# Kernel optimization log

Measured on AMD Instinct MI355X. Metric: run time of the kernel, lower is better.

Reference implementation:

```python
import jax, jax.numpy as jnp
import numpy as np

BETA = 0.25


def setup_inputs() -> dict:
    key = jax.random.key(0)
    k1, k2 = jax.random.split(key)
    x = jax.random.normal(k1, (32768, 512), dtype=jnp.float32)
    centroids = jax.random.normal(k2, (8192, 512), dtype=jnp.float32)
    return {"x": x, "centroids": centroids}


def reference(x, centroids):
    # x: [N, D], centroids: [K, D]
    x_norm = jnp.sum(x * x, axis=1, keepdims=True)          # [N, 1]
    c_norm = jnp.sum(centroids * centroids, axis=1)         # [K]
    xy = jnp.einsum('nd,kd->nk', x, centroids)              # [N, K]
    distances = x_norm + c_norm[None, :] - 2.0 * xy         # [N, K]
    indices = jnp.argmin(distances, axis=-1)                # [N]
    q = centroids[indices]                                  # [N, D] gather
    # losses: commitment = mse(sg(q), x); codebook = mse(q, sg(x))
    sg = jax.lax.stop_gradient
    commitment_loss = jnp.mean((sg(q) - x) ** 2)
    codebook_loss = jnp.mean((q - sg(x)) ** 2)
    loss = codebook_loss + BETA * commitment_loss
    # straight-through estimator
    x_q = x + sg(q - x)
    return (x_q, loss, indices)
```

## Files before the change

kernel.cpp:

```cpp
#include <hip/hip_runtime.h>
#include <hip/hip_bf16.h>

#define N_ROWS 32768
#define DIM    512
#define K_CENT 8192

#define LOSS_OFF 16777216u
#define IDX_OFF  16777217u

#define XH_OFF_B   0u
#define CH_OFF_B   33554432u
#define CN_OFF_B   41943040u
#define CAND_OFF_B 41975808u

#define CAND_BYTES 2097152u
#define CN_BYTES   32768u

#define BM 128
#define BN 128
#define KHALF 4096
#define NKT (KHALF / BN)
#define NH  2

typedef __bf16 bf16x8 __attribute__((ext_vector_type(8)));
typedef float  f32x4  __attribute__((ext_vector_type(4)));

__device__ __forceinline__ unsigned short f2bf(float f) {
    unsigned u = __float_as_uint(f);
    return (unsigned short)((u + 0x7fffu + ((u >> 16) & 1u)) >> 16);
}

__device__ __forceinline__ void glds16(void* lds, const void* g) {
    __builtin_amdgcn_global_load_lds(
        (const __attribute__((address_space(1))) unsigned*)g,
        (__attribute__((address_space(3))) unsigned*)lds, 16, 0, 0);
}

__device__ __forceinline__ void ce(float& da, int& ia, float& db, int& ib) {
    bool sw = (db < da) || (db == da && ib < ia);
    float td = sw ? db : da; int ti = sw ? ib : ia;
    float ud = sw ? da : db; int ui = sw ? ia : ib;
    da = td; ia = ti; db = ud; ib = ui;
}
__device__ __forceinline__ void lmin(float da, int ia, float db, int ib,
                                     float& od, int& oi) {
    bool sw = (db < da) || (db == da && ib < ia);
    od = sw ? db : da; oi = sw ? ib : ia;
}

__global__ void __launch_bounds__(256) convert_kernel(const float* __restrict__ x,
                                                      const float* __restrict__ c,
                                                      unsigned short* __restrict__ xh,
                                                      unsigned short* __restrict__ ch,
                                                      float* __restrict__ cnp) {
    const int wave = threadIdx.x >> 6, lane = threadIdx.x & 63;
    const int gid = blockIdx.x * 4 + wave;
    if (gid < N_ROWS) {
        const float* p = x + (size_t)gid * DIM + lane * 8;
        float4 a = *(const float4*)p, b = *(const float4*)(p + 4);
        uint4 w;
        w.x = (unsigned)f2bf(a.x) | ((unsigned)f2bf(a.y) << 16);
        w.y = (unsigned)f2bf(a.z) | ((unsigned)f2bf(a.w) << 16);
        w.z = (unsigned)f2bf(b.x) | ((unsigned)f2bf(b.y) << 16);
        w.w = (unsigned)f2bf(b.z) | ((unsigned)f2bf(b.w) << 16);
        *(uint4*)(xh + (size_t)gid * DIM + lane * 8) = w;
    } else {
        const int cr = gid - N_ROWS;
        const float* p = c + (size_t)cr * DIM + lane * 8;
        float4 a = *(const float4*)p, b = *(const float4*)(p + 4);
        uint4 w;
        w.x = (unsigned)f2bf(a.x) | ((unsigned)f2bf(a.y) << 16);
        w.y = (unsigned)f2bf(a.z) | ((unsigned)f2bf(a.w) << 16);
        w.z = (unsigned)f2bf(b.x) | ((unsigned)f2bf(b.y) << 16);
        w.w = (unsigned)f2bf(b.z) | ((unsigned)f2bf(b.w) << 16);
        *(uint4*)(ch + (size_t)cr * DIM + lane * 8) = w;
        float s = a.x*a.x + a.y*a.y + a.z*a.z + a.w*a.w
                + b.x*b.x + b.y*b.y + b.z*b.z + b.w*b.w;
#pragma unroll
        for (int off = 32; off; off >>= 1) s += __shfl_down(s, off, 64);
        if (lane == 0) cnp[cr] = s;
    }
}

__global__ void __launch_bounds__(256, 2) vq_main(const unsigned short* __restrict__ xh,
                                                  const unsigned short* __restrict__ ch,
                                                  const float* __restrict__ cnp,
                                                  float* __restrict__ cand) {
    __shared__ __align__(16) unsigned short xs[4 * 4096];
    __shared__ __align__(16) unsigned short cs[4 * 4096];
    __shared__ float sh_d[2][BM][4];
    __shared__ int   sh_i[2][BM][4];

    const int tid  = threadIdx.x;
    const int wave = tid >> 6, lane = tid & 63;
    const int wm   = wave >> 1, wk = wave & 1;
    const int lr   = lane & 15, quad = lane >> 4;
    const int nbase = blockIdx.x * BM;
    const int h     = blockIdx.y;
    const int kc0   = h * KHALF;

    const int srow16 = lane >> 2;
    const int sswz   = (lane & 3) ^ ((lane >> 3) & 3);
    const unsigned short* xg0 = xh + (size_t)(nbase + wave * 32 + srow16) * DIM + sswz * 8;
    const unsigned short* xg1 = xg0 + (size_t)16 * DIM;
    const unsigned short* cg0 = ch + (size_t)(kc0 + wave * 32 + srow16) * DIM + sswz * 8;

    unsigned short* xw = xs + wave * 1024;
    unsigned short* cw = cs + wave * 1024;

#define STAGE(ring, ktn, dd) do {                                          \
        unsigned short* xd_ = xw + (ring) * 4096;                          \
        unsigned short* cd_ = cw + (ring) * 4096;                          \
        const unsigned short* cgk_ = cg0 + (size_t)(ktn) * (BN * DIM) + (dd); \
        glds16(xd_,       xg0 + (dd));                                     \
        glds16(xd_ + 512, xg1 + (dd));                                     \
        glds16(cd_,       cgk_);                                           \
        glds16(cd_ + 512, cgk_ + 16 * DIM);                                \
    } while (0)

    int aoff[4], boff[4];
#pragma unroll
    for (int t = 0; t < 4; ++t) {
        const int sw = (quad ^ ((lr >> 1) & 3)) << 4;
        aoff[t] = (wm * 64 + t * 16 + lr) * 64 + sw;
        boff[t] = (wk * 64 + t * 16 + lr) * 64 + sw;
    }

    float rd1[4][4], rd2[4][4];
    int   ri1[4][4], ri2[4][4];
#pragma unroll
    for (int mt = 0; mt < 4; ++mt)
#pragma unroll
        for (int r = 0; r < 4; ++r) {
            rd1[mt][r] = 1e30f; rd2[mt][r] = 1e30f;
            ri1[mt][r] = 0x7ffffff0; ri2[mt][r] = 0x7ffffff1;
        }

    STAGE(0, 0, 0);
    STAGE(1, 0, 32);
    STAGE(2, 0, 64);
    asm volatile("s_waitcnt vmcnt(0)" ::: "memory");
    __builtin_amdgcn_s_barrier();

    for (int kt = 0; kt < NKT; ++kt) {
        const int kc = kc0 + kt * BN;
        float cnv[4];
#pragma unroll
        for (int t = 0; t < 4; ++t) cnv[t] = cnp[kc + wk * 64 + t * 16 + lr];

        f32x4 acc[4][4];
#pragma unroll
        for (int mt = 0; mt < 4; ++mt)
#pragma unroll
            for (int t = 0; t < 4; ++t)
                acc[mt][t] = (f32x4){0.f, 0.f, 0.f, 0.f};

#pragma unroll 4
        for (int j = 0; j < 16; ++j) {
            asm volatile("s_waitcnt vmcnt(8)" ::: "memory");
            __builtin_amdgcn_s_barrier();
            if (kt < NKT - 1 || j < 13) {
                const int jn = j + 3;
                STAGE(jn & 3, kt + (jn >> 4), (jn & 15) * 32);
            }
            const char* xb = (const char*)xs + (j & 3) * 8192;
            const char* cb = (const char*)cs + (j & 3) * 8192;
            bf16x8 bfr[4];
#pragma unroll
            for (int t = 0; t < 4; ++t)
                bfr[t] = *(const bf16x8*)(cb + boff[t]);
#pragma unroll
            for (int mt = 0; mt < 4; ++mt) {
                bf16x8 a = *(const bf16x8*)(xb + aoff[mt]);
#pragma unroll
                for (int t = 0; t < 4; ++t)
                    acc[mt][t] = __builtin_amdgcn_mfma_f32_16x16x32_bf16(a, bfr[t], acc[mt][t], 0, 0, 0);
            }
        }

#pragma unroll
        for (int t = 0; t < 4; ++t) {
            const int col = kc + wk * 64 + t * 16 + lr;
#pragma unroll
            for (int mt = 0; mt < 4; ++mt)
#pragma unroll
                for (int r = 0; r < 4; ++r) {
                    float d = fmaf(-2.f, acc[mt][t][r], cnv[t]);
                    bool b1 = d < rd1[mt][r];
                    bool b2 = d < rd2[mt][r];
                    float o1 = rd1[mt][r]; int oi1 = ri1[mt][r];
                    rd2[mt][r] = b1 ? o1 : (b2 ? d : rd2[mt][r]);
                    ri2[mt][r] = b1 ? oi1 : (b2 ? col : ri2[mt][r]);
                    rd1[mt][r] = b1 ? d : o1;
                    ri1[mt][r] = b1 ? col : oi1;
                }
        }
    }
#undef STAGE

#pragma unroll
    for (int mt = 0; mt < 4; ++mt)
#pragma unroll
        for (int r = 0; r < 4; ++r) {
            float a0 = rd1[mt][r], a1 = rd2[mt][r], a2 = 1e30f, a3 = 1e30f;
            int   i0 = ri1[mt][r], i1 = ri2[mt][r], i2 = 0x7ffffff2, i3 = 0x7ffffff3;
#pragma unroll
            for (int s = 1; s < 16; s <<= 1) {
                float p0 = __shfl_xor(a0, s, 64), p1 = __shfl_xor(a1, s, 64);
                float p2 = __shfl_xor(a2, s, 64), p3 = __shfl_xor(a3, s, 64);
                int   q0 = __shfl_xor(i0, s, 64), q1 = __shfl_xor(i1, s, 64);
                int   q2 = __shfl_xor(i2, s, 64), q3 = __shfl_xor(i3, s, 64);
                float l0, l1, l2, l3; int m0, m1, m2, m3;
                lmin(a0, i0, p3, q3, l0, m0);
                lmin(a1, i1, p2, q2, l1, m1);
                lmin(a2, i2, p1, q1, l2, m2);
                lmin(a3, i3, p0, q0, l3, m3);
                ce(l0, m0, l2, m2); ce(l1, m1, l3, m3);
                ce(l0, m0, l1, m1); ce(l2, m2, l3, m3);
                a0 = l0; a1 = l1; a2 = l2; a3 = l3;
                i0 = m0; i1 = m1; i2 = m2; i3 = m3;
            }
            if (lr == 0) {
                const int rl = wm * 64 + mt * 16 + quad * 4 + r;
                sh_d[wk][rl][0] = a0; sh_i[wk][rl][0] = i0;
                sh_d[wk][rl][1] = a1; sh_i[wk][rl][1] = i1;
                sh_d[wk][rl][2] = a2; sh_i[wk][rl][2] = i2;
                sh_d[wk][rl][3] = a3; sh_i[wk][rl][3] = i3;
            }
        }
    __syncthreads();

    if (tid < BM) {
        float a0 = sh_d[0][tid][0], a1 = sh_d[0][tid][1];
        float a2 = sh_d[0][tid][2], a3 = sh_d[0][tid][3];
        int   i0 = sh_i[0][tid][0], i1 = sh_i[0][tid][1];
        int   i2 = sh_i[0][tid][2], i3 = sh_i[0][tid][3];
        float b0 = sh_d[1][tid][0], b1 = sh_d[1][tid][1];
        float b2 = sh_d[1][tid][2], b3 = sh_d[1][tid][3];
        int   j0 = sh_i[1][tid][0], j1 = sh_i[1][tid][1];
        int   j2 = sh_i[1][tid][2], j3 = sh_i[1][tid][3];
        float l0, l1, l2, l3; int m0, m1, m2, m3;
        lmin(a0, i0, b3, j3, l0, m0);
        lmin(a1, i1, b2, j2, l1, m1);
        lmin(a2, i2, b1, j1, l2, m2);
        lmin(a3, i3, b0, j0, l3, m3);
        ce(l0, m0, l2, m2); ce(l1, m1, l3, m3);
        ce(l0, m0, l1, m1); ce(l2, m2, l3, m3);
        float* cell = cand + ((size_t)(nbase + tid) * NH + h) * 8;
        cell[0] = l0; cell[1] = (float)m0;
        cell[2] = l1; cell[3] = (float)m1;
        cell[4] = l2; cell[5] = (float)m2;
        cell[6] = l3; cell[7] = (float)m3;
    }
}

__global__ void __launch_bounds__(256) vq_refine(const float* __restrict__ x,
                                                 const float* __restrict__ cg,
                                                 const float* __restrict__ cand,
                                                 float* __restrict__ outp,
                                                 int write_xq) {
    __shared__ double ls[4];
    const int wave = threadIdx.x >> 6, lane = threadIdx.x & 63;
    const int n = blockIdx.x * 4 + wave;
    const float* cell = cand + (size_t)n * 16;
    int kid[8];
#pragma unroll
    for (int j = 0; j < 8; ++j) kid[j] = (int)cell[2 * j + 1];

    const float* xr = x + (size_t)n * DIM + lane * 8;
    float4 xa = *(const float4*)xr;
    float4 xb = *(const float4*)(xr + 4);

    float4 ca[8], cb[8];
#pragma unroll
    for (int j = 0; j < 8; ++j) {
        const float* cr = cg + (size_t)kid[j] * DIM + lane * 8;
        ca[j] = *(const float4*)cr;
        cb[j] = *(const float4*)(cr + 4);
    }

    double bd = 1e300; int bi = 0x7fffffff;
    float4 va = xa, vb = xb;
#pragma unroll
    for (int j = 0; j < 8; ++j) {
        const int k = kid[j];
        double s = 0.0, t;
        t = (double)xa.x - (double)ca[j].x; s += t * t;
        t = (double)xa.y - (double)ca[j].y; s += t * t;
        t = (double)xa.z - (double)ca[j].z; s += t * t;
        t = (double)xa.w - (double)ca[j].w; s += t * t;
        t = (double)xb.x - (double)cb[j].x; s += t * t;
        t = (double)xb.y - (double)cb[j].y; s += t * t;
        t = (double)xb.z - (double)cb[j].z; s += t * t;
        t = (double)xb.w - (double)cb[j].w; s += t * t;
#pragma unroll
        for (int off = 32; off; off >>= 1) s += __shfl_down(s, off, 64);
        s = __shfl(s, 0, 64);
        bool w = (s < bd) || (s == bd && k < bi);
        bd = w ? s : bd;
        bi = w ? k : bi;
        va.x = w ? ca[j].x : va.x; va.y = w ? ca[j].y : va.y;
        va.z = w ? ca[j].z : va.z; va.w = w ? ca[j].w : va.w;
        vb.x = w ? cb[j].x : vb.x; vb.y = w ? cb[j].y : vb.y;
        vb.z = w ? cb[j].z : vb.z; vb.w = w ? cb[j].w : vb.w;
    }
    if (write_xq) {
        float* row = outp + (size_t)n * DIM + lane * 8;
        *(float4*)row = va;
        *(float4*)(row + 4) = vb;
    }
    if (lane == 0) { outp[IDX_OFF + n] = (float)bi; ls[wave] = bd; }
    __syncthreads();
    if (threadIdx.x == 0)
        atomicAdd(outp + LOSS_OFF,
                  (float)((ls[0] + ls[1] + ls[2] + ls[3]) * (1.25 / 16777216.0)));
}

__global__ void __launch_bounds__(256) vq_gather(const float* __restrict__ cg,
                                                 float* __restrict__ outp) {
    const int wave = threadIdx.x >> 6, lane = threadIdx.x & 63;
    const int n = blockIdx.x * 4 + wave;
    const int k = (int)outp[IDX_OFF + n];
    const float* cr = cg + (size_t)k * DIM + lane * 8;
    float4 a = *(const float4*)cr;
    float4 b = *(const float4*)(cr + 4);
    float* row = outp + (size_t)n * DIM + lane * 8;
    *(float4*)row = a;
    *(float4*)(row + 4) = b;
}

extern "C" void kernel_launch(void* const* d_in, const int* in_sizes, int n_in,
                              void* d_out, int out_size, void* d_ws, size_t ws_size,
                              hipStream_t stream) {
    const float* x   = (const float*)d_in[0];
    const float* cen = (const float*)d_in[1];
    float* out = (float*)d_out;

    unsigned short* xh  = (unsigned short*)((char*)d_out + XH_OFF_B);
    unsigned short* chp = (unsigned short*)((char*)d_out + CH_OFF_B);

    const int fused = (d_ws != nullptr) && (ws_size >= (size_t)(CAND_BYTES + CN_BYTES));
    float* cand = fused ? (float*)d_ws
                        : (float*)((char*)d_out + CAND_OFF_B);
    float* cnp  = fused ? (float*)((char*)d_ws + CAND_BYTES)
                        : (float*)((char*)d_out + CN_OFF_B);

    hipMemsetAsync((void*)(out + LOSS_OFF), 0, sizeof(float), stream);
    convert_kernel<<<(N_ROWS + K_CENT) / 4, 256, 0, stream>>>(x, cen, xh, chp, cnp);
    dim3 g2(N_ROWS / BM, NH);
    vq_main<<<g2, 256, 0, stream>>>(xh, chp, cnp, cand);
    vq_refine<<<N_ROWS / 4, 256, 0, stream>>>(x, cen, cand, out, fused);
    if (!fused) vq_gather<<<N_ROWS / 4, 256, 0, stream>>>(cen, out);
}
```

Baseline: 632.0 us.

## Replace LDS-staged tiles with direct global-to-register fragment loads

Drops the shared-memory ring buffer filled by global_load_lds and instead has each wave load its MFMA A/B fragments straight from global memory into registers, double-buffered one k-step ahead. This removes the LDS traffic and most barriers, but each fragment now comes from global memory or L2 with no reuse across waves, and the loads are small strided 16-byte accesses. It also contains a redundant duplicated B load and leftover periodic barriers.

```diff
diff --git a/kernel.cpp b/kernel.cpp
--- a/kernel.cpp
+++ b/kernel.cpp
@@ -28,12 +28,6 @@
 __device__ __forceinline__ unsigned short f2bf(float f) {
     unsigned u = __float_as_uint(f);
     return (unsigned short)((u + 0x7fffu + ((u >> 16) & 1u)) >> 16);
-}
-
-__device__ __forceinline__ void glds16(void* lds, const void* g) {
-    __builtin_amdgcn_global_load_lds(
-        (const __attribute__((address_space(1))) unsigned*)g,
-        (__attribute__((address_space(3))) unsigned*)lds, 16, 0, 0);
 }
 
 __device__ __forceinline__ void ce(float& da, int& ia, float& db, int& ib) {
@@ -86,8 +80,6 @@
                                                   const unsigned short* __restrict__ ch,
                                                   const float* __restrict__ cnp,
                                                   float* __restrict__ cand) {
-    __shared__ __align__(16) unsigned short xs[4 * 4096];
-    __shared__ __align__(16) unsigned short cs[4 * 4096];
     __shared__ float sh_d[2][BM][4];
     __shared__ int   sh_i[2][BM][4];
 
@@ -99,31 +91,12 @@
     const int h     = blockIdx.y;
     const int kc0   = h * KHALF;
 
-    const int srow16 = lane >> 2;
-    const int sswz   = (lane & 3) ^ ((lane >> 3) & 3);
-    const unsigned short* xg0 = xh + (size_t)(nbase + wave * 32 + srow16) * DIM + sswz * 8;
-    const unsigned short* xg1 = xg0 + (size_t)16 * DIM;
-    const unsigned short* cg0 = ch + (size_t)(kc0 + wave * 32 + srow16) * DIM + sswz * 8;
-
-    unsigned short* xw = xs + wave * 1024;
-    unsigned short* cw = cs + wave * 1024;
-
-#define STAGE(ring, ktn, dd) do {                                          \
-        unsigned short* xd_ = xw + (ring) * 4096;                          \
-        unsigned short* cd_ = cw + (ring) * 4096;                          \
-        const unsigned short* cgk_ = cg0 + (size_t)(ktn) * (BN * DIM) + (dd); \
-        glds16(xd_,       xg0 + (dd));                                     \
-        glds16(xd_ + 512, xg1 + (dd));                                     \
-        glds16(cd_,       cgk_);                                           \
-        glds16(cd_ + 512, cgk_ + 16 * DIM);                                \
-    } while (0)
-
-    int aoff[4], boff[4];
+    const unsigned short* abase[4];
+    const unsigned short* bbase[4];
 #pragma unroll
     for (int t = 0; t < 4; ++t) {
-        const int sw = (quad ^ ((lr >> 1) & 3)) << 4;
-        aoff[t] = (wm * 64 + t * 16 + lr) * 64 + sw;
-        boff[t] = (wk * 64 + t * 16 + lr) * 64 + sw;
+        abase[t] = xh + (size_t)(nbase + wm * 64 + t * 16 + lr) * DIM + quad * 8;
+        bbase[t] = ch + (size_t)(kc0 + wk * 64 + t * 16 + lr) * DIM + quad * 8;
     }
 
     float rd1[4][4], rd2[4][4];
@@ -136,14 +109,16 @@
             ri1[mt][r] = 0x7ffffff0; ri2[mt][r] = 0x7ffffff1;
         }
 
-    STAGE(0, 0, 0);
-    STAGE(1, 0, 32);
-    STAGE(2, 0, 64);
-    asm volatile("s_waitcnt vmcnt(0)" ::: "memory");
-    __builtin_amdgcn_s_barrier();
+    bf16x8 ca[4], cb[4];
+#pragma unroll
+    for (int t = 0; t < 4; ++t) {
+        ca[t] = *(const bf16x8*)(abase[t]);
+        cb[t] = *(const bf16x8*)(bbase[t]);
+    }
 
     for (int kt = 0; kt < NKT; ++kt) {
         const int kc = kc0 + kt * BN;
+        const size_t bko = (size_t)kt * (BN * DIM);
         float cnv[4];
 #pragma unroll
         for (int t = 0; t < 4; ++t) cnv[t] = cnp[kc + wk * 64 + t * 16 + lr];
@@ -155,27 +130,37 @@
             for (int t = 0; t < 4; ++t)
                 acc[mt][t] = (f32x4){0.f, 0.f, 0.f, 0.f};
 
-#pragma unroll 4
+#pragma unroll
         for (int j = 0; j < 16; ++j) {
-            asm volatile("s_waitcnt vmcnt(8)" ::: "memory");
-            __builtin_amdgcn_s_barrier();
-            if (kt < NKT - 1 || j < 13) {
-                const int jn = j + 3;
-                STAGE(jn & 3, kt + (jn >> 4), (jn & 15) * 32);
+            bf16x8 na[4], nb[4];
+            if (j < 15) {
+                const int ko = (j + 1) * 32;
+#pragma unroll
+                for (int t = 0; t < 4; ++t) {
+                    na[t] = *(const bf16x8*)(abase[t] + ko);
+                    nb[t] = *(const bf16x8*)(bbase[t] + bko + 65536  + ko
+                                             - 65536 + (size_t)0 + 0 + (0));
+                }
+#pragma unroll
+                for (int t = 0; t < 4; ++t)
+                    nb[t] = *(const bf16x8*)(bbase[t] + bko + ko);
+            } else {
+                const int ktn = (kt + 1 < NKT) ? (kt + 1) : kt;
+                const size_t bkon = (size_t)ktn * (BN * DIM);
+#pragma unroll
+                for (int t = 0; t < 4; ++t) {
+                    na[t] = *(const bf16x8*)(abase[t]);
+                    nb[t] = *(const bf16x8*)(bbase[t] + bkon);
+                }
             }
-            const char* xb = (const char*)xs + (j & 3) * 8192;
-            const char* cb = (const char*)cs + (j & 3) * 8192;
-            bf16x8 bfr[4];
-#pragma unroll
-            for (int t = 0; t < 4; ++t)
-                bfr[t] = *(const bf16x8*)(cb + boff[t]);
-#pragma unroll
-            for (int mt = 0; mt < 4; ++mt) {
-                bf16x8 a = *(const bf16x8*)(xb + aoff[mt]);
+#pragma unroll
+            for (int mt = 0; mt < 4; ++mt)
 #pragma unroll
                 for (int t = 0; t < 4; ++t)
-                    acc[mt][t] = __builtin_amdgcn_mfma_f32_16x16x32_bf16(a, bfr[t], acc[mt][t], 0, 0, 0);
-            }
+                    acc[mt][t] = __builtin_amdgcn_mfma_f32_16x16x32_bf16(ca[mt], cb[t], acc[mt][t], 0, 0, 0);
+#pragma unroll
+            for (int t = 0; t < 4; ++t) { ca[t] = na[t]; cb[t] = nb[t]; }
+            if ((j & 3) == 3) __builtin_amdgcn_s_barrier();
         }
 
 #pragma unroll
@@ -196,7 +181,6 @@
                 }
         }
     }
-#undef STAGE
 
 #pragma unroll
     for (int mt = 0; mt < 4; ++mt)
```

Result: slower. 1.229 ms (+94.4%).

## Widen centroid tile to 256 and pack distance+index into sortable uint keys

Applied to the files above, without the earlier changes.

Doubles the centroid tile per block (BN 128→256) so each wave computes a 64x128 sub-tile, reusing A fragments across 8 B fragments. The LDS ring shrinks from 4 to 3 stages to make room for the larger tile. The running top-2 tracking and the shuffle merge network now work on single 32-bit keys instead of float/int pairs: the distance is mapped to an order-preserving unsigned, its low 13 bits are truncated and replaced by the centroid index. This cuts register pressure and the compare/select work, and halves the candidate buffer because only indices are stored. The cost is that near-tie candidates lose distance precision, which the fp32 refine pass is relied on to correct, and the larger accumulator tile may raise register pressure and lower occupancy.

```diff
diff --git a/kernel.cpp b/kernel.cpp
--- a/kernel.cpp
+++ b/kernel.cpp
@@ -13,14 +13,15 @@
 #define CN_OFF_B   41943040u
 #define CAND_OFF_B 41975808u
 
-#define CAND_BYTES 2097152u
+#define CAND_BYTES 1048576u
 #define CN_BYTES   32768u
 
 #define BM 128
-#define BN 128
+#define BN 256
 #define KHALF 4096
 #define NKT (KHALF / BN)
 #define NH  2
+#define NSTEP (NKT * 16)
 
 typedef __bf16 bf16x8 __attribute__((ext_vector_type(8)));
 typedef float  f32x4  __attribute__((ext_vector_type(4)));
@@ -29,23 +30,14 @@
     unsigned u = __float_as_uint(f);
     return (unsigned short)((u + 0x7fffu + ((u >> 16) & 1u)) >> 16);
 }
+
+__device__ __forceinline__ unsigned umn(unsigned a, unsigned b) { return a < b ? a : b; }
+__device__ __forceinline__ unsigned umx(unsigned a, unsigned b) { return a > b ? a : b; }
 
 __device__ __forceinline__ void glds16(void* lds, const void* g) {
     __builtin_amdgcn_global_load_lds(
         (const __attribute__((address_space(1))) unsigned*)g,
         (__attribute__((address_space(3))) unsigned*)lds, 16, 0, 0);
-}
-
-__device__ __forceinline__ void ce(float& da, int& ia, float& db, int& ib) {
-    bool sw = (db < da) || (db == da && ib < ia);
-    float td = sw ? db : da; int ti = sw ? ib : ia;
-    float ud = sw ? da : db; int ui = sw ? ia : ib;
-    da = td; ia = ti; db = ud; ib = ui;
-}
-__device__ __forceinline__ void lmin(float da, int ia, float db, int ib,
-                                     float& od, int& oi) {
-    bool sw = (db < da) || (db == da && ib < ia);
-    od = sw ? db : da; oi = sw ? ib : ia;
 }
 
 __global__ void __launch_bounds__(256) convert_kernel(const float* __restrict__ x,
@@ -86,10 +78,9 @@
                                                   const unsigned short* __restrict__ ch,
                                                   const float* __restrict__ cnp,
                                                   float* __restrict__ cand) {
-    __shared__ __align__(16) unsigned short xs[4 * 4096];
-    __shared__ __align__(16) unsigned short cs[4 * 4096];
-    __shared__ float sh_d[2][BM][4];
-    __shared__ int   sh_i[2][BM][4];
+    __shared__ __align__(16) unsigned short xs[3 * 4096];
+    __shared__ __align__(16) unsigned short cs[3 * 8192];
+    __shared__ unsigned sh_k[2][BM][4];
 
     const int tid  = threadIdx.x;
     const int wave = tid >> 6, lane = tid & 63;
@@ -102,97 +93,94 @@
     const int srow16 = lane >> 2;
     const int sswz   = (lane & 3) ^ ((lane >> 3) & 3);
     const unsigned short* xg0 = xh + (size_t)(nbase + wave * 32 + srow16) * DIM + sswz * 8;
-    const unsigned short* xg1 = xg0 + (size_t)16 * DIM;
-    const unsigned short* cg0 = ch + (size_t)(kc0 + wave * 32 + srow16) * DIM + sswz * 8;
+    const unsigned short* cg0 = ch + (size_t)(kc0 + wave * 64 + srow16) * DIM + sswz * 8;
 
     unsigned short* xw = xs + wave * 1024;
-    unsigned short* cw = cs + wave * 1024;
-
-#define STAGE(ring, ktn, dd) do {                                          \
-        unsigned short* xd_ = xw + (ring) * 4096;                          \
-        unsigned short* cd_ = cw + (ring) * 4096;                          \
-        const unsigned short* cgk_ = cg0 + (size_t)(ktn) * (BN * DIM) + (dd); \
-        glds16(xd_,       xg0 + (dd));                                     \
-        glds16(xd_ + 512, xg1 + (dd));                                     \
-        glds16(cd_,       cgk_);                                           \
-        glds16(cd_ + 512, cgk_ + 16 * DIM);                                \
+    unsigned short* cw = cs + wave * 2048;
+
+#define STAGE(ring, sn_) do {                                                \
+        const int ktn_ = (sn_) >> 4;                                         \
+        const int dd_  = ((sn_) & 15) * 32;                                  \
+        unsigned short* xd_ = xw + (ring) * 4096;                            \
+        unsigned short* cd_ = cw + (ring) * 8192;                            \
+        const unsigned short* xsrc_ = xg0 + dd_;                             \
+        const unsigned short* csrc_ = cg0 + (size_t)ktn_ * (BN * DIM) + dd_; \
+        glds16(xd_,        xsrc_);                                           \
+        glds16(xd_ + 512,  xsrc_ + 16 * DIM);                                \
+        glds16(cd_,        csrc_);                                           \
+        glds16(cd_ + 512,  csrc_ + 16 * DIM);                                \
+        glds16(cd_ + 1024, csrc_ + 32 * DIM);                                \
+        glds16(cd_ + 1536, csrc_ + 48 * DIM);                                \
     } while (0)
 
-    int aoff[4], boff[4];
-#pragma unroll
-    for (int t = 0; t < 4; ++t) {
-        const int sw = (quad ^ ((lr >> 1) & 3)) << 4;
-        aoff[t] = (wm * 64 + t * 16 + lr) * 64 + sw;
-        boff[t] = (wk * 64 + t * 16 + lr) * 64 + sw;
-    }
-
-    float rd1[4][4], rd2[4][4];
-    int   ri1[4][4], ri2[4][4];
+    const int sw = (quad ^ ((lr >> 1) & 3)) << 4;
+    int aoff[4], boff[8];
+#pragma unroll
+    for (int mt = 0; mt < 4; ++mt) aoff[mt] = (wm * 64 + mt * 16 + lr) * 64 + sw;
+#pragma unroll
+    for (int t = 0; t < 8; ++t)    boff[t]  = (wk * 128 + t * 16 + lr) * 64 + sw;
+
+    unsigned k1[4][4], k2[4][4];
 #pragma unroll
     for (int mt = 0; mt < 4; ++mt)
 #pragma unroll
-        for (int r = 0; r < 4; ++r) {
-            rd1[mt][r] = 1e30f; rd2[mt][r] = 1e30f;
-            ri1[mt][r] = 0x7ffffff0; ri2[mt][r] = 0x7ffffff1;
-        }
-
-    STAGE(0, 0, 0);
-    STAGE(1, 0, 32);
-    STAGE(2, 0, 64);
-    asm volatile("s_waitcnt vmcnt(0)" ::: "memory");
-    __builtin_amdgcn_s_barrier();
+        for (int r = 0; r < 4; ++r) { k1[mt][r] = 0xFFFFFFFFu; k2[mt][r] = 0xFFFFFFFFu; }
+
+    STAGE(0, 0);
+    STAGE(1, 1);
+    int rr = 0, rw = 2;
 
     for (int kt = 0; kt < NKT; ++kt) {
         const int kc = kc0 + kt * BN;
-        float cnv[4];
-#pragma unroll
-        for (int t = 0; t < 4; ++t) cnv[t] = cnp[kc + wk * 64 + t * 16 + lr];
-
-        f32x4 acc[4][4];
+        float cnv[8];
+#pragma unroll
+        for (int t = 0; t < 8; ++t) cnv[t] = cnp[kc + wk * 128 + t * 16 + lr];
+
+        f32x4 acc[4][8];
 #pragma unroll
         for (int mt = 0; mt < 4; ++mt)
 #pragma unroll
-            for (int t = 0; t < 4; ++t)
+            for (int t = 0; t < 8; ++t)
                 acc[mt][t] = (f32x4){0.f, 0.f, 0.f, 0.f};
 
-#pragma unroll 4
+#pragma unroll
         for (int j = 0; j < 16; ++j) {
-            asm volatile("s_waitcnt vmcnt(8)" ::: "memory");
+            asm volatile("s_waitcnt vmcnt(6)" ::: "memory");
             __builtin_amdgcn_s_barrier();
-            if (kt < NKT - 1 || j < 13) {
-                const int jn = j + 3;
-                STAGE(jn & 3, kt + (jn >> 4), (jn & 15) * 32);
+            int sn = kt * 16 + j + 2;
+            if (sn > NSTEP - 1) sn = NSTEP - 1;
+            STAGE(rw, sn);
+            const char* xb = (const char*)xs + rr * 8192;
+            const char* cb = (const char*)cs + rr * 16384;
+            bf16x8 af[4];
+#pragma unroll
+            for (int mt = 0; mt < 4; ++mt)
+                af[mt] = *(const bf16x8*)(xb + aoff[mt]);
+#pragma unroll
+            for (int t = 0; t < 8; ++t) {
+                bf16x8 bf = *(const bf16x8*)(cb + boff[t]);
+#pragma unroll
+                for (int mt = 0; mt < 4; ++mt)
+                    acc[mt][t] = __builtin_amdgcn_mfma_f32_16x16x32_bf16(af[mt], bf, acc[mt][t], 0, 0, 0);
             }
-            const char* xb = (const char*)xs + (j & 3) * 8192;
-            const char* cb = (const char*)cs + (j & 3) * 8192;
-            bf16x8 bfr[4];
-#pragma unroll
-            for (int t = 0; t < 4; ++t)
-                bfr[t] = *(const bf16x8*)(cb + boff[t]);
-#pragma unroll
-            for (int mt = 0; mt < 4; ++mt) {
-                bf16x8 a = *(const bf16x8*)(xb + aoff[mt]);
-#pragma unroll
-                for (int t = 0; t < 4; ++t)
-                    acc[mt][t] = __builtin_amdgcn_mfma_f32_16x16x32_bf16(a, bfr[t], acc[mt][t], 0, 0, 0);
-            }
+            rr = (rr == 2) ? 0 : rr + 1;
+            rw = (rw == 2) ? 0 : rw + 1;
         }
 
 #pragma unroll
-        for (int t = 0; t < 4; ++t) {
-            const int col = kc + wk * 64 + t * 16 + lr;
+        for (int t = 0; t < 8; ++t) {
+            const unsigned colb = (unsigned)(kc + wk * 128 + t * 16 + lr);
 #pragma unroll
             for (int mt = 0; mt < 4; ++mt)
 #pragma unroll
                 for (int r = 0; r < 4; ++r) {
                     float d = fmaf(-2.f, acc[mt][t][r], cnv[t]);
-                    bool b1 = d < rd1[mt][r];
-                    bool b2 = d < rd2[mt][r];
-                    float o1 = rd1[mt][r]; int oi1 = ri1[mt][r];
-                    rd2[mt][r] = b1 ? o1 : (b2 ? d : rd2[mt][r]);
-                    ri2[mt][r] = b1 ? oi1 : (b2 ? col : ri2[mt][r]);
-                    rd1[mt][r] = b1 ? d : o1;
-                    ri1[mt][r] = b1 ? col : oi1;
+                    unsigned u = __float_as_uint(d);
+                    u ^= ((unsigned)((int)u >> 31)) | 0x80000000u;
+                    unsigned key = (u & 0xFFFFE000u) | colb;
+                    unsigned o1 = k1[mt][r];
+                    k1[mt][r] = umn(key, o1);
+                    k2[mt][r] = umn(umx(key, o1), k2[mt][r]);
                 }
         }
     }
@@ -202,55 +190,46 @@
     for (int mt = 0; mt < 4; ++mt)
 #pragma unroll
         for (int r = 0; r < 4; ++r) {
-            float a0 = rd1[mt][r], a1 = rd2[mt][r], a2 = 1e30f, a3 = 1e30f;
-            int   i0 = ri1[mt][r], i1 = ri2[mt][r], i2 = 0x7ffffff2, i3 = 0x7ffffff3;
+            unsigned a0 = k1[mt][r], a1 = k2[mt][r];
+            unsigned a2 = 0xFFFFFFFFu, a3 = 0xFFFFFFFFu;
 #pragma unroll
             for (int s = 1; s < 16; s <<= 1) {
-                float p0 = __shfl_xor(a0, s, 64), p1 = __shfl_xor(a1, s, 64);
-                float p2 = __shfl_xor(a2, s, 64), p3 = __shfl_xor(a3, s, 64);
-                int   q0 = __shfl_xor(i0, s, 64), q1 = __shfl_xor(i1, s, 64);
-                int   q2 = __shfl_xor(i2, s, 64), q3 = __shfl_xor(i3, s, 64);
-                float l0, l1, l2, l3; int m0, m1, m2, m3;
-                lmin(a0, i0, p3, q3, l0, m0);
-                lmin(a1, i1, p2, q2, l1, m1);
-                lmin(a2, i2, p1, q1, l2, m2);
-                lmin(a3, i3, p0, q0, l3, m3);
-                ce(l0, m0, l2, m2); ce(l1, m1, l3, m3);
-                ce(l0, m0, l1, m1); ce(l2, m2, l3, m3);
-                a0 = l0; a1 = l1; a2 = l2; a3 = l3;
-                i0 = m0; i1 = m1; i2 = m2; i3 = m3;
+                unsigned p0 = (unsigned)__shfl_xor((int)a0, s, 64);
+                unsigned p1 = (unsigned)__shfl_xor((int)a1, s, 64);
+                unsigned p2 = (unsigned)__shfl_xor((int)a2, s, 64);
+                unsigned p3 = (unsigned)__shfl_xor((int)a3, s, 64);
+                unsigned l0 = umn(a0, p3), l1 = umn(a1, p2);
+                unsigned l2 = umn(a2, p1), l3 = umn(a3, p0);
+                unsigned c0 = umn(l0, l2), c2 = umx(l0, l2);
+                unsigned c1 = umn(l1, l3), c3 = umx(l1, l3);
+                a0 = umn(c0, c1); a1 = umx(c0, c1);
+                a2 = umn(c2, c3); a3 = umx(c2, c3);
             }
             if (lr == 0) {
                 const int rl = wm * 64 + mt * 16 + quad * 4 + r;
-                sh_d[wk][rl][0] = a0; sh_i[wk][rl][0] = i0;
-                sh_d[wk][rl][1] = a1; sh_i[wk][rl][1] = i1;
-                sh_d[wk][rl][2] = a2; sh_i[wk][rl][2] = i2;
-                sh_d[wk][rl][3] = a3; sh_i[wk][rl][3] = i3;
+                sh_k[wk][rl][0] = a0; sh_k[wk][rl][1] = a1;
+                sh_k[wk][rl][2] = a2; sh_k[wk][rl][3] = a3;
             }
         }
     __syncthreads();
 
     if (tid < BM) {
-        float a0 = sh_d[0][tid][0], a1 = sh_d[0][tid][1];
-        float a2 = sh_d[0][tid][2], a3 = sh_d[0][tid][3];
-        int   i0 = sh_i[0][tid][0], i1 = sh_i[0][tid][1];
-        int   i2 = sh_i[0][tid][2], i3 = sh_i[0][tid][3];
-        float b0 = sh_d[1][tid][0], b1 = sh_d[1][tid][1];
-        float b2 = sh_d[1][tid][2], b3 = sh_d[1][tid][3];
-        int   j0 = sh_i[1][tid][0], j1 = sh_i[1][tid][1];
-        int   j2 = sh_i[1][tid][2], j3 = sh_i[1][tid][3];
-        float l0, l1, l2, l3; int m0, m1, m2, m3;
-        lmin(a0, i0, b3, j3, l0, m0);
-        lmin(a1, i1, b2, j2, l1, m1);
-        lmin(a2, i2, b1, j1, l2, m2);
-        lmin(a3, i3, b0, j0, l3, m3);
-        ce(l0, m0, l2, m2); ce(l1, m1, l3, m3);
-        ce(l0, m0, l1, m1); ce(l2, m2, l3, m3);
-        float* cell = cand + ((size_t)(nbase + tid) * NH + h) * 8;
-        cell[0] = l0; cell[1] = (float)m0;
-        cell[2] = l1; cell[3] = (float)m1;
-        cell[4] = l2; cell[5] = (float)m2;
-        cell[6] = l3; cell[7] = (float)m3;
+        unsigned a0 = sh_k[0][tid][0], a1 = sh_k[0][tid][1];
+        unsigned a2 = sh_k[0][tid][2], a3 = sh_k[0][tid][3];
+        unsigned b0 = sh_k[1][tid][0], b1 = sh_k[1][tid][1];
+        unsigned b2 = sh_k[1][tid][2], b3 = sh_k[1][tid][3];
+        unsigned l0 = umn(a0, b3), l1 = umn(a1, b2);
+        unsigned l2 = umn(a2, b1), l3 = umn(a3, b0);
+        unsigned c0 = umn(l0, l2), c2 = umx(l0, l2);
+        unsigned c1 = umn(l1, l3), c3 = umx(l1, l3);
+        unsigned m0 = umn(c0, c1), m1 = umx(c0, c1);
+        unsigned m2 = umn(c2, c3), m3 = umx(c2, c3);
+        float4 v;
+        v.x = (float)(m0 & 0x1FFFu);
+        v.y = (float)(m1 & 0x1FFFu);
+        v.z = (float)(m2 & 0x1FFFu);
+        v.w = (float)(m3 & 0x1FFFu);
+        *(float4*)(cand + (size_t)(nbase + tid) * 8 + h * 4) = v;
     }
 }
 
@@ -262,10 +241,10 @@
     __shared__ double ls[4];
     const int wave = threadIdx.x >> 6, lane = threadIdx.x & 63;
     const int n = blockIdx.x * 4 + wave;
-    const float* cell = cand + (size_t)n * 16;
+    const float* cell = cand + (size_t)n * 8;
     int kid[8];
 #pragma unroll
-    for (int j = 0; j < 8; ++j) kid[j] = (int)cell[2 * j + 1];
+    for (int j = 0; j < 8; ++j) kid[j] = (int)cell[j];
 
     const float* xr = x + (size_t)n * DIM + lane * 8;
     float4 xa = *(const float4*)xr;
```

Result: slower. 690.1 us (+9.2%).
